# Performance work log

Hardware: AMD Instinct MI355X
Metric: run time of the kernel (lower is better)

The kernel has to match this reference:

```python
import jax, jax.numpy as jnp
import numpy as np

NEG_INF = -9e15  # matches torch's -9000000000000000.0 fill
ALPHA = 0.2      # LeakyReLU negative slope


def setup_inputs() -> dict:
    key = jax.random.key(0)
    k1, k2, k3, k4 = jax.random.split(key, 4)
    B, F, N, T, C = 16, 128, 256, 64, 64
    h = jax.random.normal(k1, (B, F, N, T), dtype=jnp.float32)
    adj = jax.random.randint(k2, (B, N, N), 0, 2, dtype=jnp.int32)
    W = jax.random.normal(k3, (B, F, C), dtype=jnp.float32)
    a = jax.random.normal(k4, (B, 2 * C, 1), dtype=jnp.float32)
    return {"h": h, "adj": adj, "W": W, "a": a}


def reference(h, adj, W, a):
    # Wh: (B, C, N, T)
    Wh = jnp.einsum('bfnt,bfc->bcnt', h, W)
    C = W.shape[-1]
    # The original builds the O(N^2) pairwise concat then contracts with a.
    # Equivalently: e[b,i,j,t] = leakyrelu(a1.Wh[:, i] + a2.Wh[:, j])
    a1 = a[:, :C, 0]   # (B, C)
    a2 = a[:, C:, 0]   # (B, C)
    f = jnp.einsum('bcnt,bc->bnt', Wh, a1)  # (B, N, T)
    g = jnp.einsum('bcnt,bc->bnt', Wh, a2)  # (B, N, T)
    e = jax.nn.leaky_relu(f[:, :, None, :] + g[:, None, :, :], negative_slope=ALPHA)  # (B,N,N,T)
    mask = adj[:, :, :, None] > 0  # (B, N, N, 1) broadcast over T
    e = jnp.where(mask, e, NEG_INF)
    attention = jax.nn.softmax(e, axis=2)  # softmax over neighbor index m
    # dropout = 0.0 (eval-mode reference), so skipped
    h_prime = jnp.einsum('bnmt,bcmt->bcnt', attention, Wh)
    return jax.nn.elu(h_prime)  # concat=True branch
```

## Files before the change

kernel.cpp:

```cpp
#include <hip/hip_runtime.h>

#define B_ 16
#define F_ 128
#define N_ 256
#define T_ 64
#define C_ 64
#define ALPHA_ 0.2f
#define L2E_ 1.4426950408889634f

typedef short bf16x8 __attribute__((ext_vector_type(8)));
typedef float f32x4 __attribute__((ext_vector_type(4)));

__device__ __forceinline__ unsigned short f2bf(float x){
  unsigned int u = __float_as_uint(x);
  unsigned int r = u + 0x7FFFu + ((u >> 16) & 1u);
  return (unsigned short)(r >> 16);
}
__device__ __forceinline__ unsigned pk2(float a, float b){
  return ((unsigned)f2bf(b) << 16) | (unsigned)f2bf(a);
}
__device__ __forceinline__ unsigned sbit(unsigned w, int j){
  return (unsigned)(((int)(w << (31 - j))) >> 31);
}
__device__ __forceinline__ int swzT(int c){
  return ((c & 7) ^ ((c >> 3) & 7)) << 4;
}

__global__ void k_u(const float* __restrict__ W, const float* __restrict__ a,
                    float* __restrict__ u){
  int blk = blockIdx.x, b = blk >> 2, q = blk & 3;
  int tid = threadIdx.x;
  int f = q*32 + (tid >> 3), co = (tid & 7)*8;
  const float* Wb = W + (b*F_ + f)*C_ + co;
  const float* a1 = a + b*2*C_ + co;
  const float* a2 = a1 + C_;
  float s1 = 0.f, s2 = 0.f;
#pragma unroll
  for (int c = 0; c < 8; ++c){
    float w = Wb[c];
    s1 = fmaf(w, a1[c], s1);
    s2 = fmaf(w, a2[c], s2);
  }
#pragma unroll
  for (int s = 1; s < 8; s <<= 1){
    s1 += __shfl_xor(s1, s);
    s2 += __shfl_xor(s2, s);
  }
  if ((tid & 7) == 0){
    u[b*F_ + f] = s1;
    u[B_*F_ + b*F_ + f] = s2;
  }
}

__global__ __launch_bounds__(256, 4) void k_whm(const float* __restrict__ h,
    const float* __restrict__ W, const float* __restrict__ u,
    const int* __restrict__ adj,
    unsigned short* __restrict__ wht, float* __restrict__ fvec,
    float* __restrict__ gvec, unsigned* __restrict__ amask){
  __shared__ uint4 hT4[1024];
  __shared__ uint4 wT4[1024];
  __shared__ float fpart[4][T_];
  __shared__ float gpart[4][T_];
  char* hT = (char*)hT4;
  char* wT = (char*)wT4;

  int bid = blockIdx.x;
  int tid = threadIdx.x, w = tid >> 6, l = tid & 63;

  if (bid >= B_*N_){
    int blk = bid - B_*N_;
    int b = blk >> 2, r0 = (blk & 3)*64;
    const int* ab = adj + ((size_t)b*N_ + r0 + w*16)*N_;
    unsigned* om = amask + ((size_t)b*N_ + r0 + w*16)*8;
    for (int r = 0; r < 16; ++r){
      unsigned long long m0 = __ballot(ab[r*N_ +       l] > 0);
      unsigned long long m1 = __ballot(ab[r*N_ +  64 + l] > 0);
      unsigned long long m2 = __ballot(ab[r*N_ + 128 + l] > 0);
      unsigned long long m3 = __ballot(ab[r*N_ + 192 + l] > 0);
      if (l == 0){
        *(uint4*)(om + r*8)     = make_uint4((unsigned)m0, (unsigned)(m0>>32),
                                             (unsigned)m1, (unsigned)(m1>>32));
        *(uint4*)(om + r*8 + 4) = make_uint4((unsigned)m2, (unsigned)(m2>>32),
                                             (unsigned)m3, (unsigned)(m3>>32));
      }
    }
    return;
  }

  int b = bid >> 8, n = bid & 255;
  const float* hg = h + (size_t)b*F_*N_*T_ + n*T_;
  const float* Wg = W + b*F_*C_;
  const float* u1 = u + b*F_;
  const float* u2 = u + B_*F_ + b*F_;

  float sf = 0.f, sg = 0.f;
#pragma unroll
  for (int p = 0; p < 4; ++p){
    int f0 = p*32 + w*8;
    float v[8], wv[8];
#pragma unroll
    for (int j = 0; j < 8; ++j){
      v[j]  = hg[(size_t)(f0+j)*(N_*T_) + l];
      wv[j] = Wg[(f0+j)*C_ + l];
      sf = fmaf(v[j], u1[f0+j], sf);
      sg = fmaf(v[j], u2[f0+j], sg);
    }
    uint4 ph = make_uint4(pk2(v[0],v[1]),  pk2(v[2],v[3]),  pk2(v[4],v[5]),  pk2(v[6],v[7]));
    uint4 pw = make_uint4(pk2(wv[0],wv[1]),pk2(wv[2],wv[3]),pk2(wv[4],wv[5]),pk2(wv[6],wv[7]));
    *(uint4*)(hT + ((l*256 + f0*2) ^ ((l & 7) << 4))) = ph;
    *(uint4*)(wT + ((l*256 + f0*2) ^ ((l & 7) << 4))) = pw;
  }
  fpart[w][l] = sf;
  gpart[w][l] = sg;
  __syncthreads();

  if (tid < T_){
    float f_ = (fpart[0][tid] + fpart[1][tid]) + (fpart[2][tid] + fpart[3][tid]);
    float g_ = (gpart[0][tid] + gpart[1][tid]) + (gpart[2][tid] + gpart[3][tid]);
    fvec[(b*N_ + n)*T_ + tid] = f_ * L2E_;
    gvec[(b*N_ + n)*T_ + tid] = g_ * L2E_;
  }

  int li = l & 15, g_ = l >> 4;
  bf16x8 afr[4];
#pragma unroll
  for (int ch = 0; ch < 4; ++ch){
    int c = w*16 + li;
    afr[ch] = *(bf16x8*)(wT + ((c*256 + (ch*32 + g_*8)*2) ^ ((c & 7) << 4)));
  }
  f32x4 acc[4];
#pragma unroll
  for (int tt = 0; tt < 4; ++tt) acc[tt] = (f32x4){0.f,0.f,0.f,0.f};
#pragma unroll
  for (int tt = 0; tt < 4; ++tt){
#pragma unroll
    for (int ch = 0; ch < 4; ++ch){
      int t = tt*16 + li;
      bf16x8 bfr = *(bf16x8*)(hT + ((t*256 + (ch*32 + g_*8)*2) ^ ((t & 7) << 4)));
      acc[tt] = __builtin_amdgcn_mfma_f32_16x16x32_bf16(afr[ch], bfr, acc[tt], 0, 0, 0);
    }
  }

  __syncthreads();
  char* outT = hT;
#pragma unroll
  for (int tt = 0; tt < 4; ++tt){
    int t = tt*16 + li;
    int c0 = w*16 + g_*4;
    unsigned q0 = pk2(acc[tt][0], acc[tt][1]);
    unsigned q1 = pk2(acc[tt][2], acc[tt][3]);
    *(uint2*)(outT + ((t*128 + c0*2) ^ ((t & 7) << 4))) = make_uint2(q0, q1);
  }
  __syncthreads();
  unsigned short* wb = wht + (size_t)b*T_*N_*C_ + n*C_;
#pragma unroll
  for (int k = 0; k < 2; ++k){
    int idx = tid + k*256;
    int t = idx >> 3, c8 = idx & 7;
    uint4 vq = *(const uint4*)(outT + t*128 + ((c8 ^ (t & 7)) << 4));
    *(uint4*)(wb + (size_t)t*(N_*C_) + c8*8) = vq;
  }
}

__global__ __launch_bounds__(256, 4) void k_attn(
    const unsigned short* __restrict__ wht,
    unsigned short* __restrict__ wout,
    const unsigned* __restrict__ amask,
    const float* __restrict__ fvec,
    const float* __restrict__ gvec){
  __shared__ uint4 whsT4[2048];
  __shared__ float gs[N_];
  __shared__ float fs[128];
  char* dstT = (char*)whsT4;

  int bid = blockIdx.x;
  int b = bid >> 7, t = (bid >> 1) & 63, nh = bid & 1;
  int nbase = nh*128;
  int tid = threadIdx.x, w = tid >> 6, l = tid & 63;
  int li = l & 15, g_ = l >> 4;

  gs[tid] = gvec[(b*N_ + tid)*T_ + t];
  if (tid < 128) fs[tid] = fvec[(b*N_ + nbase + tid)*T_ + t];

  uint4 mlo[2], mhi[2];
#pragma unroll
  for (int mt = 0; mt < 2; ++mt){
    int n = nbase + w*32 + mt*16 + li;
    const uint4* mp = (const uint4*)(amask + ((size_t)b*N_ + n)*8);
    mlo[mt] = mp[0];
    mhi[mt] = mp[1];
  }
  unsigned pkl[2], pkh[2];
  unsigned selA = 0x0C0C0000u | ((unsigned)(g_ + 4) << 8) | (unsigned)g_;
#pragma unroll
  for (int mt = 0; mt < 2; ++mt){
    unsigned t0 = __builtin_amdgcn_perm(mlo[mt].y, mlo[mt].x, selA);
    unsigned t1 = __builtin_amdgcn_perm(mlo[mt].w, mlo[mt].z, selA);
    pkl[mt] = __builtin_amdgcn_perm(t1, t0, 0x05040100u);
    unsigned t2 = __builtin_amdgcn_perm(mhi[mt].y, mhi[mt].x, selA);
    unsigned t3 = __builtin_amdgcn_perm(mhi[mt].w, mhi[mt].z, selA);
    pkh[mt] = __builtin_amdgcn_perm(t3, t2, 0x05040100u);
  }

  const char* src = (const char*)(wht + (size_t)(b*T_ + t)*(N_*C_));
  uint4 ra[4], rb[4];
#pragma unroll
  for (int i = 0; i < 4; ++i){
    int q2 = tid + i*256;
    int m = (q2 >> 3)*2, c0 = (q2 & 7)*8;
    ra[i] = *(const uint4*)(src + m*128 + c0*2);
    rb[i] = *(const uint4*)(src + (m+1)*128 + c0*2);
  }

  asm volatile("s_waitcnt lgkmcnt(0)" ::: "memory");
  __builtin_amdgcn_sched_barrier(0);
  __builtin_amdgcn_s_barrier();

  float fl2[2];
#pragma unroll
  for (int mt = 0; mt < 2; ++mt) fl2[mt] = fs[w*32 + mt*16 + li];

  float mg[2] = {0.f, 0.f};
#pragma unroll 1
  for (int ch = 0; ch < 8; ++ch){
    const float* gq = &gs[ch*32 + g_*8];
    float4 ga = *(const float4*)gq;
    float4 gb = *(const float4*)(gq + 4);
    float gg[8] = {ga.x, ga.y, ga.z, ga.w, gb.x, gb.y, gb.z, gb.w};
    int sh = (ch & 3)*8;
#pragma unroll
    for (int mt = 0; mt < 2; ++mt){
      unsigned wsh = ((ch & 4) ? pkh[mt] : pkl[mt]) >> sh;
      float cd[8];
#pragma unroll
      for (int j = 0; j < 8; ++j)
        cd[j] = __uint_as_float(__float_as_uint(gg[j]) & sbit(wsh, j));
      float m01 = fmaxf(cd[0], cd[1]), m23 = fmaxf(cd[2], cd[3]);
      float m45 = fmaxf(cd[4], cd[5]), m67 = fmaxf(cd[6], cd[7]);
      mg[mt] = fmaxf(mg[mt], fmaxf(fmaxf(m01, m23), fmaxf(m45, m67)));
    }
  }
  float fme[2], fme2[2];
#pragma unroll
  for (int mt = 0; mt < 2; ++mt){
    float v = mg[mt];
    v = fmaxf(v, __shfl_xor(v, 16));
    v = fmaxf(v, __shfl_xor(v, 32));
    float em = fl2[mt] + v;
    float M  = fmaxf(em, ALPHA_*em);
    fme[mt]  = fl2[mt] - M;
    fme2[mt] = fmaf(fl2[mt], ALPHA_, -M);
  }

#pragma unroll
  for (int i = 0; i < 4; ++i){
    int q2 = tid + i*256;
    int m = (q2 >> 3)*2, c0 = (q2 & 7)*8;
    unsigned va[4] = {ra[i].x, ra[i].y, ra[i].z, ra[i].w};
    unsigned vb[4] = {rb[i].x, rb[i].y, rb[i].z, rb[i].w};
#pragma unroll
    for (int k = 0; k < 4; ++k){
      int c = c0 + 2*k;
      unsigned lo = __builtin_amdgcn_perm(vb[k], va[k], 0x05040100u);
      unsigned hi = __builtin_amdgcn_perm(vb[k], va[k], 0x07060302u);
      *(unsigned*)(dstT + ((c*512 + m*2)     ^ swzT(c)))   = lo;
      *(unsigned*)(dstT + (((c+1)*512 + m*2) ^ swzT(c+1))) = hi;
    }
  }
  __syncthreads();

  bf16x8 ones;
#pragma unroll
  for (int i = 0; i < 8; ++i) ones[i] = (short)0x3F80;

  f32x4 acc[2][4], accS[2];
#pragma unroll
  for (int mt = 0; mt < 2; ++mt){
#pragma unroll
    for (int nt = 0; nt < 4; ++nt) acc[mt][nt] = (f32x4){0.f, 0.f, 0.f, 0.f};
    accS[mt] = (f32x4){0.f, 0.f, 0.f, 0.f};
  }

#pragma unroll 2
  for (int ch = 0; ch < 8; ++ch){
    bf16x8 bfr[4];
#pragma unroll
    for (int nt = 0; nt < 4; ++nt){
      int c = nt*16 + li;
      bfr[nt] = *(bf16x8*)(dstT + ((c*512 + (ch*32 + g_*8)*2) ^ swzT(c)));
    }
    const float* gq = &gs[ch*32 + g_*8];
    float4 ga = *(const float4*)gq;
    float4 gb = *(const float4*)(gq + 4);
    float gg[8] = {ga.x, ga.y, ga.z, ga.w, gb.x, gb.y, gb.z, gb.w};
    int sh = (ch & 3)*8;
#pragma unroll
    for (int mt = 0; mt < 2; ++mt){
      unsigned wsh = ((ch & 4) ? pkh[mt] : pkl[mt]) >> sh;
      float wv[8];
#pragma unroll
      for (int j = 0; j < 8; ++j){
        float d1 = gg[j] + fme[mt];
        float d2 = fmaf(gg[j], ALPHA_, fme2[mt]);
        float p  = exp2f(fmaxf(d1, d2));
        wv[j] = __uint_as_float(__float_as_uint(p) & sbit(wsh, j));
      }
      unsigned q0, q1, q2_, q3;
      asm("v_cvt_pk_bf16_f32 %0, %1, %2" : "=v"(q0)  : "v"(wv[0]), "v"(wv[1]));
      asm("v_cvt_pk_bf16_f32 %0, %1, %2" : "=v"(q1)  : "v"(wv[2]), "v"(wv[3]));
      asm("v_cvt_pk_bf16_f32 %0, %1, %2" : "=v"(q2_) : "v"(wv[4]), "v"(wv[5]));
      asm("v_cvt_pk_bf16_f32 %0, %1, %2" : "=v"(q3)  : "v"(wv[6]), "v"(wv[7]));
      union { unsigned u[4]; bf16x8 v; } afu;
      afu.u[0] = q0; afu.u[1] = q1; afu.u[2] = q2_; afu.u[3] = q3;
#pragma unroll
      for (int nt = 0; nt < 4; ++nt)
        acc[mt][nt] = __builtin_amdgcn_mfma_f32_16x16x32_bf16(afu.v, bfr[nt], acc[mt][nt], 0, 0, 0);
      accS[mt] = __builtin_amdgcn_mfma_f32_16x16x32_bf16(afu.v, ones, accS[mt], 0, 0, 0);
    }
  }

  unsigned short* ob = wout + (size_t)(b*T_ + t)*(N_*C_) + (size_t)nbase*C_;
#pragma unroll
  for (int mt = 0; mt < 2; ++mt){
#pragma unroll
    for (int reg = 0; reg < 4; ++reg){
      int rloc = w*32 + mt*16 + g_*4 + reg;
      float inv = 1.0f / accS[mt][reg];
#pragma unroll
      for (int nt = 0; nt < 4; ++nt){
        float v = acc[mt][nt][reg] * inv;
        v = v > 0.f ? v : (__expf(v) - 1.f);
        ob[rloc*C_ + nt*16 + li] = f2bf(v);
      }
    }
  }
}

__global__ __launch_bounds__(256) void k_tr(const unsigned short* __restrict__ whtO,
                                            float* __restrict__ out){
  __shared__ float tile[64][65];
  int bid = blockIdx.x;
  int b = bid >> 8, n = bid & 255;
  int tid = threadIdx.x;
  const unsigned short* src = whtO + ((size_t)b*T_*N_ + n)*C_;
#pragma unroll
  for (int i = 0; i < 2; ++i){
    int idx = tid + i*256;
    int t = idx >> 3, c0 = (idx & 7)*8;
    uint4 v = *(const uint4*)(src + (size_t)t*(N_*C_) + c0);
    unsigned arr[4] = {v.x, v.y, v.z, v.w};
#pragma unroll
    for (int k = 0; k < 4; ++k){
      tile[c0+2*k  ][t] = __uint_as_float(arr[k] << 16);
      tile[c0+2*k+1][t] = __uint_as_float(arr[k] & 0xFFFF0000u);
    }
  }
  __syncthreads();
  float* ob = out + (size_t)b*C_*N_*T_ + n*T_;
#pragma unroll
  for (int i = 0; i < 4; ++i){
    int idx = tid + i*256;
    int c = idx >> 4, t0 = (idx & 15)*4;
    float4 v = make_float4(tile[c][t0], tile[c][t0+1], tile[c][t0+2], tile[c][t0+3]);
    *(float4*)(ob + (size_t)c*(N_*T_) + t0) = v;
  }
}

extern "C" void kernel_launch(void* const* d_in, const int* in_sizes, int n_in,
                              void* d_out, int out_size, void* d_ws, size_t ws_size,
                              hipStream_t stream){
  (void)in_sizes; (void)n_in; (void)out_size; (void)ws_size;
  const float* h   = (const float*)d_in[0];
  const int*   adj = (const int*)d_in[1];
  const float* W   = (const float*)d_in[2];
  const float* a   = (const float*)d_in[3];
  float* u    = (float*)d_ws;
  float* fvec = u + 2*B_*F_;
  float* gvec = fvec + B_*N_*T_;
  unsigned short* wht = (unsigned short*)(gvec + B_*N_*T_);
  unsigned* amask = (unsigned*)(wht + (size_t)B_*T_*N_*C_);
  unsigned short* wout = (unsigned short*)(amask + (size_t)B_*N_*8);

  k_u   <<<dim3(B_*4),         dim3(256), 0, stream>>>(W, a, u);
  k_whm <<<dim3(B_*N_ + B_*4), dim3(256), 0, stream>>>(h, W, u, adj, wht, fvec, gvec, amask);
  k_attn<<<dim3(B_*T_*2),      dim3(256), 0, stream>>>(wht, wout, amask, fvec, gvec);
  k_tr  <<<dim3(B_*N_),        dim3(256), 0, stream>>>(wout, (float*)d_out);
}
```

Measured before the change: 103.5 us.

## Merge node halves into one 512-thread attention block; compute row sums in VALU

k_attn now runs one 512-thread block per (batch, time) instead of two 256-thread blocks that each staged the full Wh tile into LDS. The tile is now loaded and transposed once and shared by all 256 output rows, halving the redundant global loads and LDS staging. The softmax denominator is no longer computed by an extra MFMA against a ones vector. It is summed in fp32 registers and reduced with cross-lane shuffles, then passed through a shared inverse array. In exchange the grid has half as many blocks and each is larger, which may hurt occupancy and latency hiding, and the row sum is now taken from fp32 weights rather than the bf16-rounded ones.

```diff
diff --git a/kernel.cpp b/kernel.cpp
--- a/kernel.cpp
+++ b/kernel.cpp
@@ -162,7 +162,7 @@
   }
 }
 
-__global__ __launch_bounds__(256, 4) void k_attn(
+__global__ __launch_bounds__(512, 4) void k_attn(
     const unsigned short* __restrict__ wht,
     unsigned short* __restrict__ wout,
     const unsigned* __restrict__ amask,
@@ -170,22 +170,22 @@
     const float* __restrict__ gvec){
   __shared__ uint4 whsT4[2048];
   __shared__ float gs[N_];
-  __shared__ float fs[128];
+  __shared__ float fs[N_];
+  __shared__ float invs[N_];
   char* dstT = (char*)whsT4;
 
   int bid = blockIdx.x;
-  int b = bid >> 7, t = (bid >> 1) & 63, nh = bid & 1;
-  int nbase = nh*128;
+  int b = bid >> 6, t = bid & 63;
   int tid = threadIdx.x, w = tid >> 6, l = tid & 63;
   int li = l & 15, g_ = l >> 4;
 
-  gs[tid] = gvec[(b*N_ + tid)*T_ + t];
-  if (tid < 128) fs[tid] = fvec[(b*N_ + nbase + tid)*T_ + t];
+  if (tid < 256) gs[tid] = gvec[(b*N_ + tid)*T_ + t];
+  else           fs[tid - 256] = fvec[(b*N_ + (tid - 256))*T_ + t];
 
   uint4 mlo[2], mhi[2];
 #pragma unroll
   for (int mt = 0; mt < 2; ++mt){
-    int n = nbase + w*32 + mt*16 + li;
+    int n = w*32 + mt*16 + li;
     const uint4* mp = (const uint4*)(amask + ((size_t)b*N_ + n)*8);
     mlo[mt] = mp[0];
     mhi[mt] = mp[1];
@@ -203,10 +203,10 @@
   }
 
   const char* src = (const char*)(wht + (size_t)(b*T_ + t)*(N_*C_));
-  uint4 ra[4], rb[4];
-#pragma unroll
-  for (int i = 0; i < 4; ++i){
-    int q2 = tid + i*256;
+  uint4 ra[2], rb[2];
+#pragma unroll
+  for (int i = 0; i < 2; ++i){
+    int q2 = tid + i*512;
     int m = (q2 >> 3)*2, c0 = (q2 & 7)*8;
     ra[i] = *(const uint4*)(src + m*128 + c0*2);
     rb[i] = *(const uint4*)(src + (m+1)*128 + c0*2);
@@ -253,8 +253,8 @@
   }
 
 #pragma unroll
-  for (int i = 0; i < 4; ++i){
-    int q2 = tid + i*256;
+  for (int i = 0; i < 2; ++i){
+    int q2 = tid + i*512;
     int m = (q2 >> 3)*2, c0 = (q2 & 7)*8;
     unsigned va[4] = {ra[i].x, ra[i].y, ra[i].z, ra[i].w};
     unsigned vb[4] = {rb[i].x, rb[i].y, rb[i].z, rb[i].w};
@@ -269,17 +269,13 @@
   }
   __syncthreads();
 
-  bf16x8 ones;
-#pragma unroll
-  for (int i = 0; i < 8; ++i) ones[i] = (short)0x3F80;
-
-  f32x4 acc[2][4], accS[2];
-#pragma unroll
-  for (int mt = 0; mt < 2; ++mt){
-#pragma unroll
-    for (int nt = 0; nt < 4; ++nt) acc[mt][nt] = (f32x4){0.f, 0.f, 0.f, 0.f};
-    accS[mt] = (f32x4){0.f, 0.f, 0.f, 0.f};
-  }
+  f32x4 acc[2][4];
+#pragma unroll
+  for (int mt = 0; mt < 2; ++mt)
+#pragma unroll
+    for (int nt = 0; nt < 4; ++nt)
+      acc[mt][nt] = (f32x4){0.f, 0.f, 0.f, 0.f};
+  float s0[2] = {0.f,0.f}, s1[2] = {0.f,0.f};
 
 #pragma unroll 2
   for (int ch = 0; ch < 8; ++ch){
@@ -303,7 +299,9 @@
         float d1 = gg[j] + fme[mt];
         float d2 = fmaf(gg[j], ALPHA_, fme2[mt]);
         float p  = exp2f(fmaxf(d1, d2));
-        wv[j] = __uint_as_float(__float_as_uint(p) & sbit(wsh, j));
+        float v  = __uint_as_float(__float_as_uint(p) & sbit(wsh, j));
+        if (j < 4) s0[mt] += v; else s1[mt] += v;
+        wv[j] = v;
       }
       unsigned q0, q1, q2_, q3;
       asm("v_cvt_pk_bf16_f32 %0, %1, %2" : "=v"(q0)  : "v"(wv[0]), "v"(wv[1]));
@@ -315,17 +313,24 @@
 #pragma unroll
       for (int nt = 0; nt < 4; ++nt)
         acc[mt][nt] = __builtin_amdgcn_mfma_f32_16x16x32_bf16(afu.v, bfr[nt], acc[mt][nt], 0, 0, 0);
-      accS[mt] = __builtin_amdgcn_mfma_f32_16x16x32_bf16(afu.v, ones, accS[mt], 0, 0, 0);
-    }
-  }
-
-  unsigned short* ob = wout + (size_t)(b*T_ + t)*(N_*C_) + (size_t)nbase*C_;
+    }
+  }
+
+#pragma unroll
+  for (int mt = 0; mt < 2; ++mt){
+    float s = s0[mt] + s1[mt];
+    s += __shfl_xor(s, 16);
+    s += __shfl_xor(s, 32);
+    if (g_ == 0) invs[w*32 + mt*16 + li] = 1.0f / s;
+  }
+
+  unsigned short* ob = wout + (size_t)(b*T_ + t)*(N_*C_);
 #pragma unroll
   for (int mt = 0; mt < 2; ++mt){
 #pragma unroll
     for (int reg = 0; reg < 4; ++reg){
       int rloc = w*32 + mt*16 + g_*4 + reg;
-      float inv = 1.0f / accS[mt][reg];
+      float inv = invs[rloc];
 #pragma unroll
       for (int nt = 0; nt < 4; ++nt){
         float v = acc[mt][nt][reg] * inv;
@@ -383,6 +388,6 @@
 
   k_u   <<<dim3(B_*4),         dim3(256), 0, stream>>>(W, a, u);
   k_whm <<<dim3(B_*N_ + B_*4), dim3(256), 0, stream>>>(h, W, u, adj, wht, fvec, gvec, amask);
-  k_attn<<<dim3(B_*T_*2),      dim3(256), 0, stream>>>(wht, wout, amask, fvec, gvec);
+  k_attn<<<dim3(B_*T_),        dim3(512), 0, stream>>>(wht, wout, amask, fvec, gvec);
   k_tr  <<<dim3(B_*N_),        dim3(256), 0, stream>>>(wout, (float*)d_out);
 }
```

After: 103.7 us. About the same (+0.2%).
